# Kernel optimization log

Measured on AMD Instinct MI355X. Metric: run time of the kernel, lower is better.

Reference implementation:

```python
import jax, jax.numpy as jnp
import numpy as np

N = 25000   # num nodes
E = 500000  # num edges
B = 4       # num queries (batch)
D = 32      # hidden dim
R2 = 474    # doubled num_relation
L = 4       # num conv layers
EPS = 1e-6


def setup_inputs() -> dict:
    key = jax.random.key(0)
    ks = jax.random.split(key, 12)
    return {
        "node_in": jax.random.randint(ks[0], (E,), 0, N),
        "node_out": jax.random.randint(ks[1], (E,), 0, N),
        "relation": jax.random.randint(ks[2], (E,), 0, R2),
        "edge_weight": jnp.ones((E,), jnp.float32),
        "h_index": jax.random.randint(ks[3], (B,), 0, N),
        "r_index": jax.random.randint(ks[4], (B,), 0, R2),
        "query_embed": jax.random.normal(ks[5], (R2, D), jnp.float32) * 0.1,
        "rel_W": jax.random.normal(ks[6], (L, D, R2 * D), jnp.float32) * 0.05,
        "rel_b": jnp.zeros((L, R2 * D), jnp.float32),
        "lin_W": jax.random.normal(ks[7], (L, 13 * D, D), jnp.float32) * 0.05,
        "lin_b": jnp.zeros((L, D), jnp.float32),
        "mlp_W1": jax.random.normal(ks[8], (2 * D, 2 * D), jnp.float32) * 0.05,
        "mlp_b1": jnp.zeros((2 * D,), jnp.float32),
        "mlp_W2": jax.random.normal(ks[9], (2 * D, 1), jnp.float32) * 0.05,
        "mlp_b2": jnp.zeros((1,), jnp.float32),
    }


def _nbfnet(node_in, node_out, relation, h_index, r_index,
            edge_weight, query_embed, rel_W, rel_b, lin_W, lin_b,
            mlp_W1, mlp_b1, mlp_W2, mlp_b2):
    query = query_embed[r_index]                                   # [B, D]
    # boundary condition: query embedding placed at the head node of each query
    boundary = jnp.zeros((N, B, D), query.dtype).at[h_index, jnp.arange(B)].set(query)
    # append one self-entry per node (boundary message), as in the torch code
    node_out_ext = jnp.concatenate([node_out, jnp.arange(N)])      # [E+N]
    w_ext = jnp.concatenate([edge_weight, jnp.ones((N,), edge_weight.dtype)])[:, None, None]
    cnt = jax.ops.segment_sum(jnp.ones((E + N,), query.dtype), node_out_ext, N)[:, None, None]
    deg = jax.ops.segment_sum(edge_weight, node_out, N) + 1.0      # degree_out + 1, [N]
    scale = jnp.log(deg)
    scale = scale / scale.mean()
    scales = jnp.stack([jnp.ones_like(scale), scale, 1.0 / jnp.clip(scale, 0.01)], -1)  # [N,3]

    hidden = boundary
    for l in range(L):
        # dependent relation embeddings: [R2, B, D]
        rel_in = (query @ rel_W[l] + rel_b[l]).reshape(B, R2, D).transpose(1, 0, 2)
        # distmult message + boundary self-message: [E+N, B, D]
        msg = jnp.concatenate([rel_in[relation] * hidden[node_in], boundary], 0)
        mw = msg * w_ext
        mean = jax.ops.segment_sum(mw, node_out_ext, N) / cnt
        sq_mean = jax.ops.segment_sum(msg * mw, node_out_ext, N) / cnt
        mx = jax.ops.segment_max(mw, node_out_ext, N)
        mn = jax.ops.segment_min(mw, node_out_ext, N)
        std = jnp.sqrt(jnp.clip(sq_mean - mean * mean, EPS))
        feat = jnp.stack([mean, mx, mn, std], -1).reshape(N, B, 4 * D)   # PNA stats
        update = (feat[..., None] * scales[:, None, None, :]).reshape(N, B, 12 * D)
        hidden = jax.nn.relu(jnp.concatenate([hidden, update], -1) @ lin_W[l] + lin_b[l])

    feat = jnp.concatenate([hidden, jnp.broadcast_to(query[None], (N, B, D))], -1)  # [N,B,2D]
    h1 = jax.nn.relu(feat @ mlp_W1 + mlp_b1)
    score = (h1 @ mlp_W2 + mlp_b2)[..., 0]                          # [N, B]
    return score.T                                                  # [B, N]


def reference(node_in, node_out, relation, edge_weight, h_index, r_index,
              query_embed, rel_W, rel_b, lin_W, lin_b,
              mlp_W1, mlp_b1, mlp_W2, mlp_b2):
    return _nbfnet(node_in, node_out, relation, h_index, r_index,
                   edge_weight, query_embed, rel_W, rel_b, lin_W, lin_b,
                   mlp_W1, mlp_b1, mlp_W2, mlp_b2)
```

## Files before the change

### kernel.cpp

```cpp
#include <hip/hip_runtime.h>
#include <hip/hip_fp16.h>

#define NN  25000
#define EE  500000
#define BB  4
#define DD  32
#define LL  4
#define R2C 474
#define BD  128
#define THD 416
#define EPSF 1e-6f
#define WMH 13312

typedef _Float16 half8 __attribute__((ext_vector_type(8)));
typedef float    f32x4 __attribute__((ext_vector_type(4)));

__global__ __launch_bounds__(256) void pidx_kernel(const int* __restrict__ node_out,
                                                   int* __restrict__ cnt,
                                                   int* __restrict__ pidx) {
  int e = blockIdx.x * 256 + threadIdx.x;
  if (e < EE) pidx[e] = atomicAdd(&cnt[node_out[e]], 1);
}

__global__ __launch_bounds__(256) void prep_kernel(const int* __restrict__ cnt,
                                                   int* __restrict__ base,
                                                   float* __restrict__ cntf,
                                                   int* __restrict__ gcnt) {
  int n = blockIdx.x * 256 + threadIdx.x;
  if (n >= NN) return;
  int c = cnt[n];
  base[n] = atomicAdd(gcnt, c);
  cntf[n] = (float)(c + 1);
}

__global__ __launch_bounds__(256) void scatter_kernel(const int* __restrict__ node_in,
                                                      const int* __restrict__ node_out,
                                                      const int* __restrict__ relation,
                                                      const float* __restrict__ ew,
                                                      const int* __restrict__ base,
                                                      const int* __restrict__ pidx,
                                                      int4* __restrict__ ep) {
  int e = blockIdx.x * 256 + threadIdx.x;
  if (e >= EE) return;
  int pos = base[node_out[e]] + pidx[e];
  ep[pos] = make_int4(node_in[e], relation[e], __float_as_int(ew[e]), 0);
}

__global__ __launch_bounds__(256) void wdeg_kernel(const int* __restrict__ base,
                                                   const int* __restrict__ cnt,
                                                   const int4* __restrict__ ep,
                                                   float* __restrict__ lg,
                                                   float* __restrict__ logsum) {
  int n = blockIdx.x * 256 + threadIdx.x;
  float v = 0.f;
  if (n < NN) {
    int b = base[n], c = cnt[n];
    float s = 0.f;
    for (int p = b; p < b + c; ++p) s += __int_as_float(ep[p].z);
    v = logf(s + 1.0f);
    lg[n] = v;
  }
  __shared__ float red[256];
  red[threadIdx.x] = v; __syncthreads();
  for (int o = 128; o > 0; o >>= 1) {
    if (threadIdx.x < o) red[threadIdx.x] += red[threadIdx.x + o];
    __syncthreads();
  }
  if (threadIdx.x == 0) atomicAdd(logsum, red[0]);
}

__global__ __launch_bounds__(256) void scales_kernel(const float* __restrict__ lg,
                                                     const float* __restrict__ logsum,
                                                     float* __restrict__ scales) {
  int n = blockIdx.x * 256 + threadIdx.x;
  if (n >= NN) return;
  float mean = logsum[0] / (float)NN;
  float sc = lg[n] / mean;
  scales[n * 2 + 0] = sc;
  scales[n * 2 + 1] = 1.0f / fmaxf(sc, 0.01f);
}

__global__ __launch_bounds__(128) void init_kernel(const int* __restrict__ h_index,
                                                   const int* __restrict__ r_index,
                                                   const float* __restrict__ qemb,
                                                   float* __restrict__ query,
                                                   __half* __restrict__ h0) {
  int t = threadIdx.x; int b = t >> 5, d = t & 31;
  float qv = qemb[r_index[b] * DD + d];
  query[t] = qv;
  h0[h_index[b] * BD + t] = __float2half(qv);
}

__global__ __launch_bounds__(256) void relin_all_kernel(const float* __restrict__ query,
                                                        const float* __restrict__ relW,
                                                        const float* __restrict__ relB,
                                                        __half* __restrict__ relIn) {
  int o = blockIdx.x * 256 + threadIdx.x;
  if (o >= LL * R2C * BD) return;
  int l = o / (R2C * BD);
  int rest = o % (R2C * BD);
  int r = rest >> 7, b = (rest >> 5) & 3, d = rest & 31;
  int col = r * DD + d;
  const float* W = relW + (size_t)l * DD * R2C * DD;
  float acc = relB[(size_t)l * R2C * DD + col];
  #pragma unroll
  for (int k = 0; k < DD; ++k)
    acc = fmaf(query[b * DD + k], W[(size_t)k * (R2C * DD) + col], acc);
  relIn[o] = __float2half(acc);
}

__global__ __launch_bounds__(256) void wmbuild_kernel(const float* __restrict__ linW,
                                                      _Float16* __restrict__ Wm) {
  int idx = blockIdx.x * 256 + threadIdx.x;
  if (idx >= LL * WMH) return;
  int l = idx / WMH, rest = idx % WMH;
  int t = rest >> 10;
  int nt = (rest >> 9) & 1;
  int L = (rest >> 3) & 63;
  int j = rest & 7;
  int k = t * 32 + (L >> 4) * 8 + j;
  int n = nt * 16 + (L & 15);
  int wrow;
  if (k < 32) wrow = k;
  else {
    int kk = k - 32;
    int slab = kk >> 7, s = (kk >> 5) & 3, dd = kk & 31;
    wrow = DD + (dd * 4 + s) * 3 + slab;
  }
  Wm[idx] = (_Float16)linW[(size_t)l * THD * DD + (size_t)wrow * DD + n];
}

__global__ __launch_bounds__(256) void gather_kernel(const __half2* __restrict__ hin2,
                                                     const __half2* __restrict__ rel2,
                                                     const int4* __restrict__ ep,
                                                     const int* __restrict__ base,
                                                     const int* __restrict__ cnt,
                                                     const float* __restrict__ cntf,
                                                     const int* __restrict__ h_index,
                                                     const float* __restrict__ query,
                                                     __half2* __restrict__ statsH) {
  const int lane = threadIdx.x & 63;
  const int n = blockIdx.x * 4 + (threadIdx.x >> 6);
  const int b = lane >> 4;
  const int d0 = (lane & 15) * 2;
  const float q0 = query[b * 32 + d0], q1 = query[b * 32 + d0 + 1];
  const int hb = h_index[b];
  const int beg = __builtin_amdgcn_readfirstlane(base[n]);
  const int cnn = __builtin_amdgcn_readfirstlane(cnt[n]);
  const float mb0 = (n == hb) ? q0 : 0.f;
  const float mb1 = (n == hb) ? q1 : 0.f;
  float sa0 = mb0, qa0 = mb0 * mb0, mx0 = mb0, mn0 = mb0;
  float sa1 = mb1, qa1 = mb1 * mb1, mx1 = mb1, mn1 = mb1;

#define PROC(Ez, Hv, Rv) {                                                   \
    float w = __int_as_float(Ez);                                            \
    float2 hf = __half22float2(Hv), rf = __half22float2(Rv);                 \
    float m0 = rf.x * hf.x, mw0 = m0 * w;                                    \
    float m1 = rf.y * hf.y, mw1 = m1 * w;                                    \
    sa0 += mw0; qa0 = fmaf(m0, mw0, qa0);                                    \
    mx0 = fmaxf(mx0, mw0); mn0 = fminf(mn0, mw0);                            \
    sa1 += mw1; qa1 = fmaf(m1, mw1, qa1);                                    \
    mx1 = fmaxf(mx1, mw1); mn1 = fminf(mn1, mw1); }

  const int nb = cnn >> 2;
  if (nb > 0) {
    int4 e0 = ep[beg], e1 = ep[beg + 1], e2 = ep[beg + 2], e3 = ep[beg + 3];
    __half2 h0v = hin2[(unsigned)e0.x * 64 + lane];
    __half2 r0v = rel2[(unsigned)e0.y * 64 + lane];
    __half2 h1v = hin2[(unsigned)e1.x * 64 + lane];
    __half2 r1v = rel2[(unsigned)e1.y * 64 + lane];
    __half2 h2v = hin2[(unsigned)e2.x * 64 + lane];
    __half2 r2v = rel2[(unsigned)e2.y * 64 + lane];
    __half2 h3v = hin2[(unsigned)e3.x * 64 + lane];
    __half2 r3v = rel2[(unsigned)e3.y * 64 + lane];
    for (int it = 1; it < nb; ++it) {
      const int q = beg + it * 4;
      int4 f0 = ep[q], f1 = ep[q + 1], f2 = ep[q + 2], f3 = ep[q + 3];
      __half2 g0 = hin2[(unsigned)f0.x * 64 + lane];
      __half2 s0 = rel2[(unsigned)f0.y * 64 + lane];
      __half2 g1 = hin2[(unsigned)f1.x * 64 + lane];
      __half2 s1 = rel2[(unsigned)f1.y * 64 + lane];
      __half2 g2 = hin2[(unsigned)f2.x * 64 + lane];
      __half2 s2 = rel2[(unsigned)f2.y * 64 + lane];
      __half2 g3 = hin2[(unsigned)f3.x * 64 + lane];
      __half2 s3 = rel2[(unsigned)f3.y * 64 + lane];
      PROC(e0.z, h0v, r0v); PROC(e1.z, h1v, r1v);
      PROC(e2.z, h2v, r2v); PROC(e3.z, h3v, r3v);
      e0 = f0; e1 = f1; e2 = f2; e3 = f3;
      h0v = g0; h1v = g1; h2v = g2; h3v = g3;
      r0v = s0; r1v = s1; r2v = s2; r3v = s3;
    }
    PROC(e0.z, h0v, r0v); PROC(e1.z, h1v, r1v);
    PROC(e2.z, h2v, r2v); PROC(e3.z, h3v, r3v);
  }
  for (int p = beg + (nb << 2); p < beg + cnn; ++p) {
    int4 e = ep[p];
    __half2 hv = hin2[(unsigned)e.x * 64 + lane];
    __half2 rv = rel2[(unsigned)e.y * 64 + lane];
    PROC(e.z, hv, rv);
  }
#undef PROC
  const float invc = 1.0f / cntf[n];
  const float mean0 = sa0 * invc, mean1 = sa1 * invc;
  const float sd0 = sqrtf(fmaxf(qa0 * invc - mean0 * mean0, EPSF));
  const float sd1 = sqrtf(fmaxf(qa1 * invc - mean1 * mean1, EPSF));
  __half2* sp = statsH + (unsigned)n * 256 + lane;
  sp[0]   = __floats2half2_rn(mean0, mean1);
  sp[64]  = __floats2half2_rn(mx0, mx1);
  sp[128] = __floats2half2_rn(mn0, mn1);
  sp[192] = __floats2half2_rn(sd0, sd1);
}

__global__ __launch_bounds__(128) void mfma_linear_kernel(const _Float16* __restrict__ hinh,
                                                          __half* __restrict__ houth,
                                                          const _Float16* __restrict__ statsH,
                                                          const float* __restrict__ scales,
                                                          const _Float16* __restrict__ Wm,
                                                          const float* __restrict__ bias) {
  const int lane = threadIdx.x & 63;
  const int wid  = threadIdx.x >> 6;
  const int nbase = blockIdx.x * 8 + wid * 4;
  const int m = lane & 15;
  const int q = lane >> 4;
  const int n = nbase + (m >> 2);
  const int b = m & 3;
  const _Float16 one = (_Float16)1.f;
  const _Float16 s1h = (_Float16)scales[n * 2 + 0];
  const _Float16 s2h = (_Float16)scales[n * 2 + 1];
  const _Float16* hsrc = hinh   + (unsigned)n * BD  + b * 32 + q * 8;
  const _Float16* ssrc = statsH + (unsigned)n * 512 + b * 32 + q * 8;

  f32x4 c0 = {0.f, 0.f, 0.f, 0.f};
  f32x4 c1 = {0.f, 0.f, 0.f, 0.f};
  #pragma unroll
  for (int t = 0; t < 13; ++t) {
    half8 a;
    if (t == 0) {
      a = *(const half8*)hsrc;
    } else {
      const int slab = (t - 1) >> 2, s = (t - 1) & 3;
      a = *(const half8*)(ssrc + s * 128);
      const _Float16 sc = (slab == 0) ? one : ((slab == 1) ? s1h : s2h);
      half8 sv = {sc, sc, sc, sc, sc, sc, sc, sc};
      a = a * sv;
    }
    half8 b0 = *(const half8*)(Wm + (unsigned)(t * 2 + 0) * 512 + lane * 8);
    half8 b1 = *(const half8*)(Wm + (unsigned)(t * 2 + 1) * 512 + lane * 8);
    c0 = __builtin_amdgcn_mfma_f32_16x16x32_f16(a, b0, c0, 0, 0, 0);
    c1 = __builtin_amdgcn_mfma_f32_16x16x32_f16(a, b1, c1, 0, 0, 0);
  }
  const int col = lane & 15;
  const float bj0 = bias[col], bj1 = bias[col + 16];
  #pragma unroll
  for (int i = 0; i < 4; ++i) {
    const int mr = q * 4 + i;
    const int nl = mr >> 2, bq = mr & 3;
    __half* dst = houth + (unsigned)(nbase + nl) * BD + bq * 32 + col;
    dst[0]  = __float2half(fmaxf(c0[i] + bj0, 0.f));
    dst[16] = __float2half(fmaxf(c1[i] + bj1, 0.f));
  }
}

__global__ __launch_bounds__(128) void mlp_kernel(const __half* __restrict__ hinh,
                                                  const float* __restrict__ query,
                                                  const float* __restrict__ W1,
                                                  const float* __restrict__ b1,
                                                  const float* __restrict__ W2,
                                                  const float* __restrict__ b2,
                                                  float* __restrict__ out) {
  __shared__ float f2[BB][2 * DD];
  const int t = threadIdx.x;
  const int b = t >> 5, d = t & 31;
  const float qv = query[t];
  const float w2a = W2[d], w2b = W2[DD + d];
  const float b1a = b1[d], b1b = b1[DD + d];
  const float b2v = b2[0];
  const int NPBM = 8;
  int n0 = blockIdx.x * NPBM, n1 = min(n0 + NPBM, NN);
  for (int n = n0; n < n1; ++n) {
    f2[b][d]      = __half2float(hinh[(unsigned)n * BD + t]);
    f2[b][DD + d] = qv;
    float a0 = b1a, a1 = b1b;
    #pragma unroll
    for (int i = 0; i < 2 * DD; ++i) {
      float v = f2[b][i];
      a0 = fmaf(v, W1[i * 2 * DD + d], a0);
      a1 = fmaf(v, W1[i * 2 * DD + DD + d], a1);
    }
    a0 = fmaxf(a0, 0.f); a1 = fmaxf(a1, 0.f);
    float part = a0 * w2a + a1 * w2b;
    #pragma unroll
    for (int off = 16; off > 0; off >>= 1) part += __shfl_down(part, off, 32);
    if (d == 0) out[b * NN + n] = part + b2v;
  }
}

extern "C" void kernel_launch(void* const* d_in, const int* in_sizes, int n_in,
                              void* d_out, int out_size, void* d_ws, size_t ws_size,
                              hipStream_t stream) {
  const int*   node_in  = (const int*)d_in[0];
  const int*   node_out = (const int*)d_in[1];
  const int*   relation = (const int*)d_in[2];
  const float* ew       = (const float*)d_in[3];
  const int*   h_index  = (const int*)d_in[4];
  const int*   r_index  = (const int*)d_in[5];
  const float* qemb     = (const float*)d_in[6];
  const float* relW     = (const float*)d_in[7];
  const float* relB     = (const float*)d_in[8];
  const float* linW     = (const float*)d_in[9];
  const float* linB     = (const float*)d_in[10];
  const float* W1       = (const float*)d_in[11];
  const float* b1       = (const float*)d_in[12];
  const float* W2       = (const float*)d_in[13];
  const float* b2       = (const float*)d_in[14];
  float* out = (float*)d_out;

  char* ws = (char*)d_ws;
  size_t off = 0;
  auto alloc = [&](size_t bytes) -> char* {
    char* p = ws + off;
    off += (bytes + 255) & ~(size_t)255;
    return p;
  };
  __half*   h0     = (__half*)  alloc((size_t)NN * BD * 2);
  __half*   h1     = (__half*)  alloc((size_t)NN * BD * 2);
  __half*   relIn  = (__half*)  alloc((size_t)LL * R2C * BD * 2);
  __half*   statsH = (__half*)  alloc((size_t)NN * 512 * 2);
  _Float16* Wm     = (_Float16*)alloc((size_t)LL * WMH * 2);
  int4*     ep     = (int4*)    alloc((size_t)EE * 16);
  int*      pidx   = (int*)     alloc((size_t)EE * 4);
  int*      base   = (int*)     alloc((size_t)NN * 4);
  int*      cnti   = (int*)     alloc((size_t)NN * 4);
  float*    lg     = (float*)   alloc((size_t)NN * 4);
  float*    cntf   = (float*)   alloc((size_t)NN * 4);
  float*    scales = (float*)   alloc((size_t)NN * 2 * 4);
  float*    query  = (float*)   alloc((size_t)BD * 4);
  float*    stats  = (float*)   alloc(256);

  hipMemsetAsync(cnti, 0, (size_t)NN * 4, stream);
  hipMemsetAsync(stats, 0, 256, stream);
  hipMemsetAsync(h0,   0, (size_t)NN * BD * 2, stream);

  float* logsum = stats;
  int*   gcnt   = (int*)stats + 1;

  pidx_kernel   <<<(EE + 255) / 256, 256, 0, stream>>>(node_out, cnti, pidx);
  prep_kernel   <<<(NN + 255) / 256, 256, 0, stream>>>(cnti, base, cntf, gcnt);
  scatter_kernel<<<(EE + 255) / 256, 256, 0, stream>>>(node_in, node_out, relation, ew,
                                                       base, pidx, ep);
  wdeg_kernel   <<<(NN + 255) / 256, 256, 0, stream>>>(base, cnti, ep, lg, logsum);
  scales_kernel <<<(NN + 255) / 256, 256, 0, stream>>>(lg, logsum, scales);
  init_kernel   <<<1, 128, 0, stream>>>(h_index, r_index, qemb, query, h0);
  wmbuild_kernel<<<(LL * WMH + 255) / 256, 256, 0, stream>>>(linW, Wm);
  relin_all_kernel<<<(LL * R2C * BD + 255) / 256, 256, 0, stream>>>(query, relW, relB, relIn);

  __half* hin = h0; __half* hout = h1;
  for (int l = 0; l < LL; ++l) {
    gather_kernel<<<NN / 4, 256, 0, stream>>>(
        (const __half2*)hin, (const __half2*)relIn + (size_t)l * R2C * 64,
        ep, base, cnti, cntf, h_index, query, (__half2*)statsH);
    mfma_linear_kernel<<<NN / 8, 128, 0, stream>>>(
        (const _Float16*)hin, hout, (const _Float16*)statsH, scales,
        Wm + (size_t)l * WMH, linB + (size_t)l * DD);
    __half* tmp = hin; hin = hout; hout = tmp;
  }
  mlp_kernel<<<(NN + 7) / 8, 128, 0, stream>>>(hin, query, W1, b1, W2, b2, out);
}
```

Baseline: 329.0 us.

## Pack edge records into 8-byte int2 and deepen gather prefetch to eight edges

Edge records shrink from int4 (16 bytes) to int2 by packing node_in (15 bits) and relation into one word, with the weight in the other. This halves CSR edge traffic in the gather and degree kernels. The gather loop now prefetches eight edges' rows per iteration instead of four, with 4-wide and scalar tails, to hide more gather latency. The cost is higher register pressure, which can lower occupancy, and per-node segments are padded to even sizes, which enlarges the edge buffer.

```diff
diff --git a/kernel.cpp b/kernel.cpp
--- a/kernel.cpp
+++ b/kernel.cpp
@@ -29,7 +29,7 @@
   int n = blockIdx.x * 256 + threadIdx.x;
   if (n >= NN) return;
   int c = cnt[n];
-  base[n] = atomicAdd(gcnt, c);
+  base[n] = atomicAdd(gcnt, (c + 1) & ~1);
   cntf[n] = (float)(c + 1);
 }
 
@@ -39,16 +39,16 @@
                                                       const float* __restrict__ ew,
                                                       const int* __restrict__ base,
                                                       const int* __restrict__ pidx,
-                                                      int4* __restrict__ ep) {
+                                                      int2* __restrict__ ep) {
   int e = blockIdx.x * 256 + threadIdx.x;
   if (e >= EE) return;
   int pos = base[node_out[e]] + pidx[e];
-  ep[pos] = make_int4(node_in[e], relation[e], __float_as_int(ew[e]), 0);
+  ep[pos] = make_int2(node_in[e] | (relation[e] << 15), __float_as_int(ew[e]));
 }
 
 __global__ __launch_bounds__(256) void wdeg_kernel(const int* __restrict__ base,
                                                    const int* __restrict__ cnt,
-                                                   const int4* __restrict__ ep,
+                                                   const int2* __restrict__ ep,
                                                    float* __restrict__ lg,
                                                    float* __restrict__ logsum) {
   int n = blockIdx.x * 256 + threadIdx.x;
@@ -56,7 +56,7 @@
   if (n < NN) {
     int b = base[n], c = cnt[n];
     float s = 0.f;
-    for (int p = b; p < b + c; ++p) s += __int_as_float(ep[p].z);
+    for (int p = b; p < b + c; ++p) s += __int_as_float(ep[p].y);
     v = logf(s + 1.0f);
     lg[n] = v;
   }
@@ -132,7 +132,7 @@
 
 __global__ __launch_bounds__(256) void gather_kernel(const __half2* __restrict__ hin2,
                                                      const __half2* __restrict__ rel2,
-                                                     const int4* __restrict__ ep,
+                                                     const int2* __restrict__ ep,
                                                      const int* __restrict__ base,
                                                      const int* __restrict__ cnt,
                                                      const float* __restrict__ cntf,
@@ -161,44 +161,55 @@
     mx0 = fmaxf(mx0, mw0); mn0 = fminf(mn0, mw0);                            \
     sa1 += mw1; qa1 = fmaf(m1, mw1, qa1);                                    \
     mx1 = fmaxf(mx1, mw1); mn1 = fminf(mn1, mw1); }
-
-  const int nb = cnn >> 2;
+#define ROWS(Ex, Hd, Rd) {                                                   \
+    Hd = hin2[(unsigned)((Ex) & 0x7fff) * 64 + lane];                        \
+    Rd = rel2[(unsigned)((unsigned)(Ex) >> 15) * 64 + lane]; }
+
+  int p = beg;
+  int rem = cnn;
+  const int nb = rem >> 3;
   if (nb > 0) {
-    int4 e0 = ep[beg], e1 = ep[beg + 1], e2 = ep[beg + 2], e3 = ep[beg + 3];
-    __half2 h0v = hin2[(unsigned)e0.x * 64 + lane];
-    __half2 r0v = rel2[(unsigned)e0.y * 64 + lane];
-    __half2 h1v = hin2[(unsigned)e1.x * 64 + lane];
-    __half2 r1v = rel2[(unsigned)e1.y * 64 + lane];
-    __half2 h2v = hin2[(unsigned)e2.x * 64 + lane];
-    __half2 r2v = rel2[(unsigned)e2.y * 64 + lane];
-    __half2 h3v = hin2[(unsigned)e3.x * 64 + lane];
-    __half2 r3v = rel2[(unsigned)e3.y * 64 + lane];
+    int2 E0, E1, E2, E3, E4, E5, E6, E7;
+    __half2 H0, H1, H2, H3, H4, H5, H6, H7;
+    __half2 R0, R1, R2, R3, R4, R5, R6, R7;
+    E0 = ep[p];     E1 = ep[p + 1]; E2 = ep[p + 2]; E3 = ep[p + 3];
+    E4 = ep[p + 4]; E5 = ep[p + 5]; E6 = ep[p + 6]; E7 = ep[p + 7];
+    ROWS(E0.x, H0, R0); ROWS(E1.x, H1, R1); ROWS(E2.x, H2, R2); ROWS(E3.x, H3, R3);
+    ROWS(E4.x, H4, R4); ROWS(E5.x, H5, R5); ROWS(E6.x, H6, R6); ROWS(E7.x, H7, R7);
     for (int it = 1; it < nb; ++it) {
-      const int q = beg + it * 4;
-      int4 f0 = ep[q], f1 = ep[q + 1], f2 = ep[q + 2], f3 = ep[q + 3];
-      __half2 g0 = hin2[(unsigned)f0.x * 64 + lane];
-      __half2 s0 = rel2[(unsigned)f0.y * 64 + lane];
-      __half2 g1 = hin2[(unsigned)f1.x * 64 + lane];
-      __half2 s1 = rel2[(unsigned)f1.y * 64 + lane];
-      __half2 g2 = hin2[(unsigned)f2.x * 64 + lane];
-      __half2 s2 = rel2[(unsigned)f2.y * 64 + lane];
-      __half2 g3 = hin2[(unsigned)f3.x * 64 + lane];
-      __half2 s3 = rel2[(unsigned)f3.y * 64 + lane];
-      PROC(e0.z, h0v, r0v); PROC(e1.z, h1v, r1v);
-      PROC(e2.z, h2v, r2v); PROC(e3.z, h3v, r3v);
-      e0 = f0; e1 = f1; e2 = f2; e3 = f3;
-      h0v = g0; h1v = g1; h2v = g2; h3v = g3;
-      r0v = s0; r1v = s1; r2v = s2; r3v = s3;
+      const int pn = p + 8;
+      int2 F0 = ep[pn],     F1 = ep[pn + 1], F2 = ep[pn + 2], F3 = ep[pn + 3];
+      int2 F4 = ep[pn + 4], F5 = ep[pn + 5], F6 = ep[pn + 6], F7 = ep[pn + 7];
+      __half2 G0, G1, G2, G3, G4, G5, G6, G7;
+      __half2 S0, S1, S2, S3, S4, S5, S6, S7;
+      ROWS(F0.x, G0, S0); ROWS(F1.x, G1, S1); ROWS(F2.x, G2, S2); ROWS(F3.x, G3, S3);
+      ROWS(F4.x, G4, S4); ROWS(F5.x, G5, S5); ROWS(F6.x, G6, S6); ROWS(F7.x, G7, S7);
+      PROC(E0.y, H0, R0); PROC(E1.y, H1, R1); PROC(E2.y, H2, R2); PROC(E3.y, H3, R3);
+      PROC(E4.y, H4, R4); PROC(E5.y, H5, R5); PROC(E6.y, H6, R6); PROC(E7.y, H7, R7);
+      E0 = F0; E1 = F1; E2 = F2; E3 = F3; E4 = F4; E5 = F5; E6 = F6; E7 = F7;
+      H0 = G0; H1 = G1; H2 = G2; H3 = G3; H4 = G4; H5 = G5; H6 = G6; H7 = G7;
+      R0 = S0; R1 = S1; R2 = S2; R3 = S3; R4 = S4; R5 = S5; R6 = S6; R7 = S7;
+      p = pn;
     }
-    PROC(e0.z, h0v, r0v); PROC(e1.z, h1v, r1v);
-    PROC(e2.z, h2v, r2v); PROC(e3.z, h3v, r3v);
-  }
-  for (int p = beg + (nb << 2); p < beg + cnn; ++p) {
-    int4 e = ep[p];
-    __half2 hv = hin2[(unsigned)e.x * 64 + lane];
-    __half2 rv = rel2[(unsigned)e.y * 64 + lane];
-    PROC(e.z, hv, rv);
-  }
+    PROC(E0.y, H0, R0); PROC(E1.y, H1, R1); PROC(E2.y, H2, R2); PROC(E3.y, H3, R3);
+    PROC(E4.y, H4, R4); PROC(E5.y, H5, R5); PROC(E6.y, H6, R6); PROC(E7.y, H7, R7);
+    p += 8;
+    rem -= nb << 3;
+  }
+  if (rem >= 4) {
+    int2 E0 = ep[p], E1 = ep[p + 1], E2 = ep[p + 2], E3 = ep[p + 3];
+    __half2 H0, H1, H2, H3, R0, R1, R2, R3;
+    ROWS(E0.x, H0, R0); ROWS(E1.x, H1, R1); ROWS(E2.x, H2, R2); ROWS(E3.x, H3, R3);
+    PROC(E0.y, H0, R0); PROC(E1.y, H1, R1); PROC(E2.y, H2, R2); PROC(E3.y, H3, R3);
+    p += 4; rem -= 4;
+  }
+  for (; rem > 0; --rem, ++p) {
+    int2 e = ep[p];
+    __half2 hv, rv;
+    ROWS(e.x, hv, rv);
+    PROC(e.y, hv, rv);
+  }
+#undef ROWS
 #undef PROC
   const float invc = 1.0f / cntf[n];
   const float mean0 = sa0 * invc, mean1 = sa1 * invc;
@@ -327,7 +338,7 @@
   __half*   relIn  = (__half*)  alloc((size_t)LL * R2C * BD * 2);
   __half*   statsH = (__half*)  alloc((size_t)NN * 512 * 2);
   _Float16* Wm     = (_Float16*)alloc((size_t)LL * WMH * 2);
-  int4*     ep     = (int4*)    alloc((size_t)EE * 16);
+  int2*     ep     = (int2*)    alloc(((size_t)EE + NN) * 8);
   int*      pidx   = (int*)     alloc((size_t)EE * 4);
   int*      base   = (int*)     alloc((size_t)NN * 4);
   int*      cnti   = (int*)     alloc((size_t)NN * 4);
```

After: 313.4 us. 4.7% less time.
